# Performance work log

Measured on AMD Instinct MI355X. Metric: run time of the kernel, lower is better.

## Reference

```python
import jax, jax.numpy as jnp
import numpy as np

EPS = 1e-10


def _make_spd(key, shape):
    # entrywise-nonnegative SPD: B>=0 -> B@B^T has nonnegative entries and is PSD;
    # + c*I keeps it well-conditioned and entrywise nonnegative.
    B = jax.random.uniform(key, shape, dtype=jnp.float32)
    D = jnp.einsum('...ij,...kj->...ik', B, B)
    return D + 0.05 * jnp.eye(3, dtype=jnp.float32)


def setup_inputs() -> dict:
    key = jax.random.key(0)
    k1, k2 = jax.random.split(key)
    shape = (2, 128, 128, 64, 3, 3)
    return {"D1": _make_spd(k1, shape), "D2": _make_spd(k2, shape)}


def _log_spd(D):
    # sanitize like torch.nan_to_num(..., nan=eps, posinf=eps, neginf=eps)
    D = jnp.nan_to_num(D, nan=EPS, posinf=EPS, neginf=EPS)
    D = jnp.abs(D)  # entrywise abs; input is symmetric so abs stays symmetric
    w, V = jnp.linalg.eigh(D)            # [...,3], [...,3,3]
    lw = jnp.log(w + EPS) + EPS
    # V @ diag(lw) @ V^T
    return jnp.einsum('...ij,...j,...kj->...ik', V, lw, V)


def reference(D1, D2):
    diff = _log_spd(D1) - _log_spd(D2)
    return jnp.mean(diff * diff)
```

## Files before the change

kernel.cpp:

```cpp
#include <hip/hip_runtime.h>
#include <math.h>

#define EPS_F 1e-10f

typedef __attribute__((ext_vector_type(2))) float f2;
typedef __attribute__((ext_vector_type(2))) unsigned int u2;

__device__ __forceinline__ f2 v_fabs(f2 x) {
  u2 u = __builtin_bit_cast(u2, x);
  u &= 0x7fffffffu;
  return __builtin_bit_cast(f2, u);
}
__device__ __forceinline__ f2 v_max(f2 a, f2 b) { return __builtin_elementwise_max(a, b); }
__device__ __forceinline__ f2 v_min(f2 a, f2 b) { return __builtin_elementwise_min(a, b); }
__device__ __forceinline__ f2 v_log(f2 x) {
  f2 r; r.x = __logf(x.x); r.y = __logf(x.y); return r;
}
__device__ __forceinline__ f2 v_rcp(f2 x) {
  f2 r; r.x = __builtin_amdgcn_rcpf(x.x); r.y = __builtin_amdgcn_rcpf(x.y); return r;
}
__device__ __forceinline__ f2 v_sqrt(f2 x) {
  f2 r; r.x = __builtin_amdgcn_sqrtf(x.x); r.y = __builtin_amdgcn_sqrtf(x.y); return r;
}
__device__ __forceinline__ f2 v_cos(f2 x) {
  f2 r; r.x = __cosf(x.x); r.y = __cosf(x.y); return r;
}

__device__ __forceinline__ f2 v_san(f2 v) {
  f2 a = v_fabs(v);
  f2 r;
  r.x = (a.x <= __FLT_MAX__) ? a.x : EPS_F;
  r.y = (a.y <= __FLT_MAX__) ? a.y : EPS_F;
  return r;
}

__device__ __forceinline__ f2 v_acos(f2 r) {
  const f2 t = v_fabs(r);
  const f2 s = v_sqrt(1.0f - t);
  f2 p = f2{-0.0012624911f, -0.0012624911f};
  p = p * t +  0.0066700901f;
  p = p * t + -0.0170881256f;
  p = p * t +  0.0308918810f;
  p = p * t + -0.0501743046f;
  p = p * t +  0.0889789874f;
  p = p * t + -0.2145988016f;
  p = p * t +  1.5707963050f;
  const f2 ac = s * p;
  f2 res;
  res.x = (r.x < 0.0f) ? (3.14159265358979f - ac.x) : ac.x;
  res.y = (r.y < 0.0f) ? (3.14159265358979f - ac.y) : ac.y;
  return res;
}

__device__ __forceinline__ float pair_loss(f2 a00, f2 a01, f2 a02,
                                           f2 a11, f2 a12, f2 a22) {
  const f2 q   = (a00 + a11 + a22) * (1.0f / 3.0f);
  const f2 b00 = a00 - q, b11 = a11 - q, b22 = a22 - q;
  const f2 p2  = b00 * b00 + b11 * b11 + b22 * b22 +
                 2.0f * (a01 * a01 + a02 * a02 + a12 * a12);

  f2 p = v_sqrt(p2 * (1.0f / 6.0f));
  p = v_max(p, 1e-5f * q + 1e-35f);

  const f2 pinv = v_rcp(p);
  const f2 detB = b00 * (b11 * b22 - a12 * a12)
                - a01 * (a01 * b22 - a12 * a02)
                + a02 * (a01 * a12 - b11 * a02);
  f2 r = detB * 0.5f * pinv * pinv * pinv;
  r = v_min(f2{1.0f, 1.0f}, v_max(f2{-1.0f, -1.0f}, r));
  const f2 phi  = v_acos(r) * (1.0f / 3.0f);
  const f2 twop = 2.0f * p;
  const f2 l1 = q + twop * v_cos(phi);
  const f2 l3 = q + twop * v_cos(phi + 2.0943951023931953f);
  const f2 l2 = 3.0f * q - l1 - l3;

  const f2 s00 = a00 * a00 + a01 * a01 + a02 * a02;
  const f2 s01 = a00 * a01 + a01 * a11 + a02 * a12;
  const f2 s02 = a00 * a02 + a01 * a12 + a02 * a22;
  const f2 s11 = a01 * a01 + a11 * a11 + a12 * a12;
  const f2 s12 = a01 * a02 + a11 * a12 + a12 * a22;
  const f2 s22 = a02 * a02 + a12 * a12 + a22 * a22;

  const f2 g12 = l1 - l2, g23 = l2 - l3;
  f2 alpha, gamma;
  alpha.x = (g12.x >= g23.x) ? l1.x : l3.x;
  gamma.x = (g12.x >= g23.x) ? l3.x : l1.x;
  alpha.y = (g12.y >= g23.y) ? l1.y : l3.y;
  gamma.y = (g12.y >= g23.y) ? l3.y : l1.y;
  const f2 beta = l2;

  const f2 f_a = v_log(alpha + EPS_F) + EPS_F;
  const f2 f_b = v_log(beta  + EPS_F) + EPS_F;
  const f2 f_g = v_log(gamma + EPS_F) + EPS_F;

  const f2 inv_den_a = v_rcp((alpha - beta) * (alpha - gamma));
  const f2 sbg = beta + gamma, pbg = beta * gamma;

  const f2 sab = alpha + beta, pab = alpha * beta;

  const f2 gap = gamma - beta;
  const f2 ga  = gamma - alpha;
  const f2 agap = v_fabs(gap);
  const f2 thr  = 1e-5f * v_max(v_fabs(beta), v_fabs(gamma));
  const f2 mid  = 0.5f * (beta + gamma) + EPS_F;
  f2 num, den;
  num.x = (agap.x > thr.x) ? (f_g.x - f_b.x) : 1.0f;
  den.x = (agap.x > thr.x) ? (gap.x * ga.x) : (mid.x * ga.x);
  num.y = (agap.y > thr.y) ? (f_g.y - f_b.y) : 1.0f;
  den.y = (agap.y > thr.y) ? (gap.y * ga.y) : (mid.y * ga.y);
  const f2 cg = num * v_rcp(den);

  const f2 w = f_a - f_b;
  const f2 wd = w * inv_den_a;

  const f2 L0 = f_b + wd * (s00 - sbg * a00 + pbg) + cg * (s00 - sab * a00 + pab);
  const f2 L1 =       wd * (s01 - sbg * a01)       + cg * (s01 - sab * a01);
  const f2 L2 =       wd * (s02 - sbg * a02)       + cg * (s02 - sab * a02);
  const f2 L3 = f_b + wd * (s11 - sbg * a11 + pbg) + cg * (s11 - sab * a11 + pab);
  const f2 L4 =       wd * (s12 - sbg * a12)       + cg * (s12 - sab * a12);
  const f2 L5 = f_b + wd * (s22 - sbg * a22 + pbg) + cg * (s22 - sab * a22 + pab);

  const float d0 = L0.x - L0.y;
  const float d1 = L1.x - L1.y;
  const float d2 = L2.x - L2.y;
  const float d3 = L3.x - L3.y;
  const float d4 = L4.x - L4.y;
  const float d5 = L5.x - L5.y;
  return d0 * d0 + d3 * d3 + d5 * d5 + 2.0f * (d1 * d1 + d2 * d2 + d4 * d4);
}

#define PAIRS_PER_CHUNK 256
#define FLOATS_PER_CHUNK (PAIRS_PER_CHUNK * 9)

__global__ void __launch_bounds__(256)
leloss_partial(const float* __restrict__ d1, const float* __restrict__ d2,
               float* __restrict__ partial, int nmat, int nchunk) {
  __shared__ float sA[FLOATS_PER_CHUNK];
  __shared__ float sB[FLOATS_PER_CHUNK];

  const int tid = threadIdx.x;
  float acc = 0.0f;

  for (int c = blockIdx.x; c < nchunk; c += gridDim.x) {
    const int base = c * PAIRS_PER_CHUNK;
    const int rem  = nmat - base;

    if (rem >= PAIRS_PER_CHUNK) {
      const float4* g1 = reinterpret_cast<const float4*>(d1 + (size_t)base * 9);
      const float4* g2 = reinterpret_cast<const float4*>(d2 + (size_t)base * 9);
      float4* s4A = reinterpret_cast<float4*>(sA);
      float4* s4B = reinterpret_cast<float4*>(sB);
#pragma unroll
      for (int k = 0; k < FLOATS_PER_CHUNK / 4 / 256 + 1; ++k) {
        const int idx = tid + k * 256;
        if (idx < FLOATS_PER_CHUNK / 4) { s4A[idx] = g1[idx]; s4B[idx] = g2[idx]; }
      }
    } else {
      const int nflt = rem * 9;
      for (int k = tid; k < nflt; k += 256) {
        sA[k] = d1[(size_t)base * 9 + k];
        sB[k] = d2[(size_t)base * 9 + k];
      }
    }
    __syncthreads();

    if (tid < rem) {
      const int o = tid * 9;
      const f2 m00 = v_san(f2{sA[o + 0], sB[o + 0]});
      const f2 m01 = v_san(f2{sA[o + 1], sB[o + 1]});
      const f2 m02 = v_san(f2{sA[o + 2], sB[o + 2]});
      const f2 m11 = v_san(f2{sA[o + 4], sB[o + 4]});
      const f2 m12 = v_san(f2{sA[o + 5], sB[o + 5]});
      const f2 m22 = v_san(f2{sA[o + 8], sB[o + 8]});
      acc += pair_loss(m00, m01, m02, m11, m12, m22);
    }
    __syncthreads();
  }

#pragma unroll
  for (int off = 32; off > 0; off >>= 1) acc += __shfl_down(acc, off, 64);

  __shared__ float wsum[4];
  const int lane = tid & 63;
  const int wid  = tid >> 6;
  if (lane == 0) wsum[wid] = acc;
  __syncthreads();
  if (tid == 0) {
    partial[blockIdx.x] = wsum[0] + wsum[1] + wsum[2] + wsum[3];
  }
}

__global__ void __launch_bounds__(256)
leloss_reduce(const float* __restrict__ partial, int n,
              float* __restrict__ out, double inv_count) {
  double s = 0.0;
  for (int i = threadIdx.x; i < n; i += 256) s += (double)partial[i];
#pragma unroll
  for (int off = 32; off > 0; off >>= 1) s += __shfl_down(s, off, 64);

  __shared__ double wsum[4];
  const int lane = threadIdx.x & 63;
  const int wid  = threadIdx.x >> 6;
  if (lane == 0) wsum[wid] = s;
  __syncthreads();
  if (threadIdx.x == 0) {
    const double total = wsum[0] + wsum[1] + wsum[2] + wsum[3];
    out[0] = (float)(total * inv_count);
  }
}

extern "C" void kernel_launch(void* const* d_in, const int* in_sizes, int n_in,
                              void* d_out, int out_size, void* d_ws, size_t ws_size,
                              hipStream_t stream) {
  const float* d1 = (const float*)d_in[0];
  const float* d2 = (const float*)d_in[1];
  float* out = (float*)d_out;
  float* partial = (float*)d_ws;

  const long long nelem = (long long)in_sizes[0];
  const int nmat   = (int)(nelem / 9);
  const int nchunk = (nmat + PAIRS_PER_CHUNK - 1) / PAIRS_PER_CHUNK;
  const int nblocks = nchunk < 2048 ? nchunk : 2048;

  leloss_partial<<<nblocks, 256, 0, stream>>>(d1, d2, partial, nmat, nchunk);

  const double inv_count = 1.0 / ((double)nmat * 9.0);
  leloss_reduce<<<1, 256, 0, stream>>>(partial, nblocks, out, inv_count);
}
```

Baseline: 33.65 us.

## Load tiles with direct global-to-LDS copies and process two matrix pairs per thread

```diff
diff --git a/kernel.cpp b/kernel.cpp
--- a/kernel.cpp
+++ b/kernel.cpp
@@ -3,41 +3,53 @@
 
 #define EPS_F 1e-10f
 
+typedef __attribute__((ext_vector_type(4))) float f4;
+typedef __attribute__((ext_vector_type(4))) unsigned int u4;
 typedef __attribute__((ext_vector_type(2))) float f2;
-typedef __attribute__((ext_vector_type(2))) unsigned int u2;
-
-__device__ __forceinline__ f2 v_fabs(f2 x) {
-  u2 u = __builtin_bit_cast(u2, x);
+
+typedef const __attribute__((address_space(1))) float4* gv4p;
+typedef __attribute__((address_space(3))) float4* lv4p;
+
+__device__ __forceinline__ f4 v_fabs(f4 x) {
+  u4 u = __builtin_bit_cast(u4, x);
   u &= 0x7fffffffu;
-  return __builtin_bit_cast(f2, u);
-}
-__device__ __forceinline__ f2 v_max(f2 a, f2 b) { return __builtin_elementwise_max(a, b); }
-__device__ __forceinline__ f2 v_min(f2 a, f2 b) { return __builtin_elementwise_min(a, b); }
-__device__ __forceinline__ f2 v_log(f2 x) {
-  f2 r; r.x = __logf(x.x); r.y = __logf(x.y); return r;
-}
-__device__ __forceinline__ f2 v_rcp(f2 x) {
-  f2 r; r.x = __builtin_amdgcn_rcpf(x.x); r.y = __builtin_amdgcn_rcpf(x.y); return r;
-}
-__device__ __forceinline__ f2 v_sqrt(f2 x) {
-  f2 r; r.x = __builtin_amdgcn_sqrtf(x.x); r.y = __builtin_amdgcn_sqrtf(x.y); return r;
-}
-__device__ __forceinline__ f2 v_cos(f2 x) {
-  f2 r; r.x = __cosf(x.x); r.y = __cosf(x.y); return r;
-}
-
-__device__ __forceinline__ f2 v_san(f2 v) {
-  f2 a = v_fabs(v);
-  f2 r;
+  return __builtin_bit_cast(f4, u);
+}
+__device__ __forceinline__ f4 v_max(f4 a, f4 b) { return __builtin_elementwise_max(a, b); }
+__device__ __forceinline__ f4 v_min(f4 a, f4 b) { return __builtin_elementwise_min(a, b); }
+__device__ __forceinline__ f4 v_log(f4 x) {
+  f4 r; r.x = __logf(x.x); r.y = __logf(x.y); r.z = __logf(x.z); r.w = __logf(x.w); return r;
+}
+__device__ __forceinline__ f4 v_rcp(f4 x) {
+  f4 r;
+  r.x = __builtin_amdgcn_rcpf(x.x); r.y = __builtin_amdgcn_rcpf(x.y);
+  r.z = __builtin_amdgcn_rcpf(x.z); r.w = __builtin_amdgcn_rcpf(x.w);
+  return r;
+}
+__device__ __forceinline__ f4 v_sqrt(f4 x) {
+  f4 r;
+  r.x = __builtin_amdgcn_sqrtf(x.x); r.y = __builtin_amdgcn_sqrtf(x.y);
+  r.z = __builtin_amdgcn_sqrtf(x.z); r.w = __builtin_amdgcn_sqrtf(x.w);
+  return r;
+}
+__device__ __forceinline__ f4 v_cos(f4 x) {
+  f4 r; r.x = __cosf(x.x); r.y = __cosf(x.y); r.z = __cosf(x.z); r.w = __cosf(x.w); return r;
+}
+
+__device__ __forceinline__ f4 v_san(f4 v) {
+  f4 a = v_fabs(v);
+  f4 r;
   r.x = (a.x <= __FLT_MAX__) ? a.x : EPS_F;
   r.y = (a.y <= __FLT_MAX__) ? a.y : EPS_F;
+  r.z = (a.z <= __FLT_MAX__) ? a.z : EPS_F;
+  r.w = (a.w <= __FLT_MAX__) ? a.w : EPS_F;
   return r;
 }
 
-__device__ __forceinline__ f2 v_acos(f2 r) {
-  const f2 t = v_fabs(r);
-  const f2 s = v_sqrt(1.0f - t);
-  f2 p = f2{-0.0012624911f, -0.0012624911f};
+__device__ __forceinline__ f4 v_acos(f4 r) {
+  const f4 t = v_fabs(r);
+  const f4 s = v_sqrt(1.0f - t);
+  f4 p = f4{-0.0012624911f, -0.0012624911f, -0.0012624911f, -0.0012624911f};
   p = p * t +  0.0066700901f;
   p = p * t + -0.0170881256f;
   p = p * t +  0.0308918810f;
@@ -45,115 +57,126 @@
   p = p * t +  0.0889789874f;
   p = p * t + -0.2145988016f;
   p = p * t +  1.5707963050f;
-  const f2 ac = s * p;
-  f2 res;
+  const f4 ac = s * p;
+  f4 res;
   res.x = (r.x < 0.0f) ? (3.14159265358979f - ac.x) : ac.x;
   res.y = (r.y < 0.0f) ? (3.14159265358979f - ac.y) : ac.y;
+  res.z = (r.z < 0.0f) ? (3.14159265358979f - ac.z) : ac.z;
+  res.w = (r.w < 0.0f) ? (3.14159265358979f - ac.w) : ac.w;
   return res;
 }
 
-__device__ __forceinline__ float pair_loss(f2 a00, f2 a01, f2 a02,
-                                           f2 a11, f2 a12, f2 a22) {
-  const f2 q   = (a00 + a11 + a22) * (1.0f / 3.0f);
-  const f2 b00 = a00 - q, b11 = a11 - q, b22 = a22 - q;
-  const f2 p2  = b00 * b00 + b11 * b11 + b22 * b22 +
+__device__ __forceinline__ f2 pair_loss(f4 a00, f4 a01, f4 a02,
+                                        f4 a11, f4 a12, f4 a22) {
+  const f4 q   = (a00 + a11 + a22) * (1.0f / 3.0f);
+  const f4 b00 = a00 - q, b11 = a11 - q, b22 = a22 - q;
+  const f4 p2  = b00 * b00 + b11 * b11 + b22 * b22 +
                  2.0f * (a01 * a01 + a02 * a02 + a12 * a12);
 
-  f2 p = v_sqrt(p2 * (1.0f / 6.0f));
+  f4 p = v_sqrt(p2 * (1.0f / 6.0f));
   p = v_max(p, 1e-5f * q + 1e-35f);
 
-  const f2 pinv = v_rcp(p);
-  const f2 detB = b00 * (b11 * b22 - a12 * a12)
+  const f4 pinv = v_rcp(p);
+  const f4 detB = b00 * (b11 * b22 - a12 * a12)
                 - a01 * (a01 * b22 - a12 * a02)
                 + a02 * (a01 * a12 - b11 * a02);
-  f2 r = detB * 0.5f * pinv * pinv * pinv;
-  r = v_min(f2{1.0f, 1.0f}, v_max(f2{-1.0f, -1.0f}, r));
-  const f2 phi  = v_acos(r) * (1.0f / 3.0f);
-  const f2 twop = 2.0f * p;
-  const f2 l1 = q + twop * v_cos(phi);
-  const f2 l3 = q + twop * v_cos(phi + 2.0943951023931953f);
-  const f2 l2 = 3.0f * q - l1 - l3;
-
-  const f2 s00 = a00 * a00 + a01 * a01 + a02 * a02;
-  const f2 s01 = a00 * a01 + a01 * a11 + a02 * a12;
-  const f2 s02 = a00 * a02 + a01 * a12 + a02 * a22;
-  const f2 s11 = a01 * a01 + a11 * a11 + a12 * a12;
-  const f2 s12 = a01 * a02 + a11 * a12 + a12 * a22;
-  const f2 s22 = a02 * a02 + a12 * a12 + a22 * a22;
-
-  const f2 g12 = l1 - l2, g23 = l2 - l3;
-  f2 alpha, gamma;
-  alpha.x = (g12.x >= g23.x) ? l1.x : l3.x;
-  gamma.x = (g12.x >= g23.x) ? l3.x : l1.x;
-  alpha.y = (g12.y >= g23.y) ? l1.y : l3.y;
-  gamma.y = (g12.y >= g23.y) ? l3.y : l1.y;
-  const f2 beta = l2;
-
-  const f2 f_a = v_log(alpha + EPS_F) + EPS_F;
-  const f2 f_b = v_log(beta  + EPS_F) + EPS_F;
-  const f2 f_g = v_log(gamma + EPS_F) + EPS_F;
-
-  const f2 inv_den_a = v_rcp((alpha - beta) * (alpha - gamma));
-  const f2 sbg = beta + gamma, pbg = beta * gamma;
-
-  const f2 sab = alpha + beta, pab = alpha * beta;
-
-  const f2 gap = gamma - beta;
-  const f2 ga  = gamma - alpha;
-  const f2 agap = v_fabs(gap);
-  const f2 thr  = 1e-5f * v_max(v_fabs(beta), v_fabs(gamma));
-  const f2 mid  = 0.5f * (beta + gamma) + EPS_F;
-  f2 num, den;
+  f4 r = detB * 0.5f * pinv * pinv * pinv;
+  r = v_min(f4{1.0f, 1.0f, 1.0f, 1.0f}, v_max(f4{-1.0f, -1.0f, -1.0f, -1.0f}, r));
+  const f4 phi  = v_acos(r) * (1.0f / 3.0f);
+  const f4 twop = 2.0f * p;
+  const f4 l1 = q + twop * v_cos(phi);
+  const f4 l3 = q + twop * v_cos(phi + 2.0943951023931953f);
+  const f4 l2 = 3.0f * q - l1 - l3;
+
+  const f4 s00 = a00 * a00 + a01 * a01 + a02 * a02;
+  const f4 s01 = a00 * a01 + a01 * a11 + a02 * a12;
+  const f4 s02 = a00 * a02 + a01 * a12 + a02 * a22;
+  const f4 s11 = a01 * a01 + a11 * a11 + a12 * a12;
+  const f4 s12 = a01 * a02 + a11 * a12 + a12 * a22;
+  const f4 s22 = a02 * a02 + a12 * a12 + a22 * a22;
+
+  const f4 g12 = l1 - l2, g23 = l2 - l3;
+  f4 alpha, gamma;
+  alpha.x = (g12.x >= g23.x) ? l1.x : l3.x;  gamma.x = (g12.x >= g23.x) ? l3.x : l1.x;
+  alpha.y = (g12.y >= g23.y) ? l1.y : l3.y;  gamma.y = (g12.y >= g23.y) ? l3.y : l1.y;
+  alpha.z = (g12.z >= g23.z) ? l1.z : l3.z;  gamma.z = (g12.z >= g23.z) ? l3.z : l1.z;
+  alpha.w = (g12.w >= g23.w) ? l1.w : l3.w;  gamma.w = (g12.w >= g23.w) ? l3.w : l1.w;
+  const f4 beta = l2;
+
+  const f4 f_a = v_log(alpha + EPS_F) + EPS_F;
+  const f4 f_b = v_log(beta  + EPS_F) + EPS_F;
+  const f4 f_g = v_log(gamma + EPS_F) + EPS_F;
+
+  const f4 inv_den_a = v_rcp((alpha - beta) * (alpha - gamma));
+  const f4 sbg = beta + gamma, pbg = beta * gamma;
+  const f4 sab = alpha + beta, pab = alpha * beta;
+
+  const f4 gap = gamma - beta;
+  const f4 ga  = gamma - alpha;
+  const f4 agap = v_fabs(gap);
+  const f4 thr  = 1e-5f * v_max(v_fabs(beta), v_fabs(gamma));
+  const f4 mid  = 0.5f * (beta + gamma) + EPS_F;
+  f4 num, den;
   num.x = (agap.x > thr.x) ? (f_g.x - f_b.x) : 1.0f;
   den.x = (agap.x > thr.x) ? (gap.x * ga.x) : (mid.x * ga.x);
   num.y = (agap.y > thr.y) ? (f_g.y - f_b.y) : 1.0f;
   den.y = (agap.y > thr.y) ? (gap.y * ga.y) : (mid.y * ga.y);
-  const f2 cg = num * v_rcp(den);
-
-  const f2 w = f_a - f_b;
-  const f2 wd = w * inv_den_a;
-
-  const f2 L0 = f_b + wd * (s00 - sbg * a00 + pbg) + cg * (s00 - sab * a00 + pab);
-  const f2 L1 =       wd * (s01 - sbg * a01)       + cg * (s01 - sab * a01);
-  const f2 L2 =       wd * (s02 - sbg * a02)       + cg * (s02 - sab * a02);
-  const f2 L3 = f_b + wd * (s11 - sbg * a11 + pbg) + cg * (s11 - sab * a11 + pab);
-  const f2 L4 =       wd * (s12 - sbg * a12)       + cg * (s12 - sab * a12);
-  const f2 L5 = f_b + wd * (s22 - sbg * a22 + pbg) + cg * (s22 - sab * a22 + pab);
-
-  const float d0 = L0.x - L0.y;
-  const float d1 = L1.x - L1.y;
-  const float d2 = L2.x - L2.y;
-  const float d3 = L3.x - L3.y;
-  const float d4 = L4.x - L4.y;
-  const float d5 = L5.x - L5.y;
-  return d0 * d0 + d3 * d3 + d5 * d5 + 2.0f * (d1 * d1 + d2 * d2 + d4 * d4);
-}
-
-#define PAIRS_PER_CHUNK 256
-#define FLOATS_PER_CHUNK (PAIRS_PER_CHUNK * 9)
-
-__global__ void __launch_bounds__(256)
+  num.z = (agap.z > thr.z) ? (f_g.z - f_b.z) : 1.0f;
+  den.z = (agap.z > thr.z) ? (gap.z * ga.z) : (mid.z * ga.z);
+  num.w = (agap.w > thr.w) ? (f_g.w - f_b.w) : 1.0f;
+  den.w = (agap.w > thr.w) ? (gap.w * ga.w) : (mid.w * ga.w);
+  const f4 cg = num * v_rcp(den);
+
+  const f4 wd = (f_a - f_b) * inv_den_a;
+
+  const f4 L0 = f_b + wd * (s00 - sbg * a00 + pbg) + cg * (s00 - sab * a00 + pab);
+  const f4 L1 =       wd * (s01 - sbg * a01)       + cg * (s01 - sab * a01);
+  const f4 L2 =       wd * (s02 - sbg * a02)       + cg * (s02 - sab * a02);
+  const f4 L3 = f_b + wd * (s11 - sbg * a11 + pbg) + cg * (s11 - sab * a11 + pab);
+  const f4 L4 =       wd * (s12 - sbg * a12)       + cg * (s12 - sab * a12);
+  const f4 L5 = f_b + wd * (s22 - sbg * a22 + pbg) + cg * (s22 - sab * a22 + pab);
+
+  const float dA0 = L0.x - L0.y, dB0 = L0.z - L0.w;
+  const float dA1 = L1.x - L1.y, dB1 = L1.z - L1.w;
+  const float dA2 = L2.x - L2.y, dB2 = L2.z - L2.w;
+  const float dA3 = L3.x - L3.y, dB3 = L3.z - L3.w;
+  const float dA4 = L4.x - L4.y, dB4 = L4.z - L4.w;
+  const float dA5 = L5.x - L5.y, dB5 = L5.z - L5.w;
+  f2 out;
+  out.x = dA0 * dA0 + dA3 * dA3 + dA5 * dA5 + 2.0f * (dA1 * dA1 + dA2 * dA2 + dA4 * dA4);
+  out.y = dB0 * dB0 + dB3 * dB3 + dB5 * dB5 + 2.0f * (dB1 * dB1 + dB2 * dB2 + dB4 * dB4);
+  return out;
+}
+
+#define CHUNK 512
+#define CHUNK_FLOATS (CHUNK * 9)
+#define CHUNK_V4 (CHUNK_FLOATS / 4)
+
+__global__ void __launch_bounds__(256, 4)
 leloss_partial(const float* __restrict__ d1, const float* __restrict__ d2,
                float* __restrict__ partial, int nmat, int nchunk) {
-  __shared__ float sA[FLOATS_PER_CHUNK];
-  __shared__ float sB[FLOATS_PER_CHUNK];
+  __shared__ float sA[CHUNK_FLOATS];
+  __shared__ float sB[CHUNK_FLOATS];
 
   const int tid = threadIdx.x;
   float acc = 0.0f;
 
   for (int c = blockIdx.x; c < nchunk; c += gridDim.x) {
-    const int base = c * PAIRS_PER_CHUNK;
+    const int base = c * CHUNK;
     const int rem  = nmat - base;
 
-    if (rem >= PAIRS_PER_CHUNK) {
+    if (rem >= CHUNK) {
       const float4* g1 = reinterpret_cast<const float4*>(d1 + (size_t)base * 9);
       const float4* g2 = reinterpret_cast<const float4*>(d2 + (size_t)base * 9);
       float4* s4A = reinterpret_cast<float4*>(sA);
       float4* s4B = reinterpret_cast<float4*>(sB);
 #pragma unroll
-      for (int k = 0; k < FLOATS_PER_CHUNK / 4 / 256 + 1; ++k) {
+      for (int k = 0; k < 5; ++k) {
         const int idx = tid + k * 256;
-        if (idx < FLOATS_PER_CHUNK / 4) { s4A[idx] = g1[idx]; s4B[idx] = g2[idx]; }
+        if (idx < CHUNK_V4) {
+          __builtin_amdgcn_global_load_lds((gv4p)(g1 + idx), (lv4p)(s4A + idx), 16, 0, 0);
+          __builtin_amdgcn_global_load_lds((gv4p)(g2 + idx), (lv4p)(s4B + idx), 16, 0, 0);
+        }
       }
     } else {
       const int nflt = rem * 9;
@@ -164,15 +187,18 @@
     }
     __syncthreads();
 
-    if (tid < rem) {
-      const int o = tid * 9;
-      const f2 m00 = v_san(f2{sA[o + 0], sB[o + 0]});
-      const f2 m01 = v_san(f2{sA[o + 1], sB[o + 1]});
-      const f2 m02 = v_san(f2{sA[o + 2], sB[o + 2]});
-      const f2 m11 = v_san(f2{sA[o + 4], sB[o + 4]});
-      const f2 m12 = v_san(f2{sA[o + 5], sB[o + 5]});
-      const f2 m22 = v_san(f2{sA[o + 8], sB[o + 8]});
-      acc += pair_loss(m00, m01, m02, m11, m12, m22);
+    {
+      const int ia = min(tid, rem - 1);
+      const int ib = min(tid + 256, rem - 1);
+      const int oa = ia * 9, ob = ib * 9;
+      const f4 m00 = v_san(f4{sA[oa + 0], sB[oa + 0], sA[ob + 0], sB[ob + 0]});
+      const f4 m01 = v_san(f4{sA[oa + 1], sB[oa + 1], sA[ob + 1], sB[ob + 1]});
+      const f4 m02 = v_san(f4{sA[oa + 2], sB[oa + 2], sA[ob + 2], sB[ob + 2]});
+      const f4 m11 = v_san(f4{sA[oa + 4], sB[oa + 4], sA[ob + 4], sB[ob + 4]});
+      const f4 m12 = v_san(f4{sA[oa + 5], sB[oa + 5], sA[ob + 5], sB[ob + 5]});
+      const f4 m22 = v_san(f4{sA[oa + 8], sB[oa + 8], sA[ob + 8], sB[ob + 8]});
+      const f2 l = pair_loss(m00, m01, m02, m11, m12, m22);
+      acc += (tid < rem ? l.x : 0.0f) + (tid + 256 < rem ? l.y : 0.0f);
     }
     __syncthreads();
   }
@@ -219,7 +245,7 @@
 
   const long long nelem = (long long)in_sizes[0];
   const int nmat   = (int)(nelem / 9);
-  const int nchunk = (nmat + PAIRS_PER_CHUNK - 1) / PAIRS_PER_CHUNK;
+  const int nchunk = (nmat + CHUNK - 1) / CHUNK;
   const int nblocks = nchunk < 2048 ? nchunk : 2048;
 
   leloss_partial<<<nblocks, 256, 0, stream>>>(d1, d2, partial, nmat, nchunk);
```

Measured after the change: 35.16 us. 1.04x slower.

## Use per-wave direct global-to-LDS loads and simplify log-matrix reconstruction

Applied to the files above, without the earlier changes.

```diff
diff --git a/kernel.cpp b/kernel.cpp
--- a/kernel.cpp
+++ b/kernel.cpp
@@ -5,6 +5,9 @@
 
 typedef __attribute__((ext_vector_type(2))) float f2;
 typedef __attribute__((ext_vector_type(2))) unsigned int u2;
+
+typedef const __attribute__((address_space(1))) char* gcp;
+typedef __attribute__((address_space(3))) char* lcp;
 
 __device__ __forceinline__ f2 v_fabs(f2 x) {
   u2 u = __builtin_bit_cast(u2, x);
@@ -19,19 +22,14 @@
 __device__ __forceinline__ f2 v_rcp(f2 x) {
   f2 r; r.x = __builtin_amdgcn_rcpf(x.x); r.y = __builtin_amdgcn_rcpf(x.y); return r;
 }
+__device__ __forceinline__ f2 v_rsq(f2 x) {
+  f2 r; r.x = __builtin_amdgcn_rsqf(x.x); r.y = __builtin_amdgcn_rsqf(x.y); return r;
+}
 __device__ __forceinline__ f2 v_sqrt(f2 x) {
   f2 r; r.x = __builtin_amdgcn_sqrtf(x.x); r.y = __builtin_amdgcn_sqrtf(x.y); return r;
 }
 __device__ __forceinline__ f2 v_cos(f2 x) {
   f2 r; r.x = __cosf(x.x); r.y = __cosf(x.y); return r;
-}
-
-__device__ __forceinline__ f2 v_san(f2 v) {
-  f2 a = v_fabs(v);
-  f2 r;
-  r.x = (a.x <= __FLT_MAX__) ? a.x : EPS_F;
-  r.y = (a.y <= __FLT_MAX__) ? a.y : EPS_F;
-  return r;
 }
 
 __device__ __forceinline__ f2 v_acos(f2 r) {
@@ -54,15 +52,18 @@
 
 __device__ __forceinline__ float pair_loss(f2 a00, f2 a01, f2 a02,
                                            f2 a11, f2 a12, f2 a22) {
+  a00 = v_fabs(a00); a01 = v_fabs(a01); a02 = v_fabs(a02);
+  a11 = v_fabs(a11); a12 = v_fabs(a12); a22 = v_fabs(a22);
+
   const f2 q   = (a00 + a11 + a22) * (1.0f / 3.0f);
   const f2 b00 = a00 - q, b11 = a11 - q, b22 = a22 - q;
   const f2 p2  = b00 * b00 + b11 * b11 + b22 * b22 +
                  2.0f * (a01 * a01 + a02 * a02 + a12 * a12);
 
-  f2 p = v_sqrt(p2 * (1.0f / 6.0f));
-  p = v_max(p, 1e-5f * q + 1e-35f);
-
-  const f2 pinv = v_rcp(p);
+  const f2 p2c  = v_max(p2 * (1.0f / 6.0f), 1e-10f * q * q + 1e-35f);
+  const f2 pinv = v_rsq(p2c);
+  const f2 p    = p2c * pinv;
+
   const f2 detB = b00 * (b11 * b22 - a12 * a12)
                 - a01 * (a01 * b22 - a12 * a02)
                 + a02 * (a01 * a12 - b11 * a02);
@@ -83,20 +84,15 @@
 
   const f2 g12 = l1 - l2, g23 = l2 - l3;
   f2 alpha, gamma;
-  alpha.x = (g12.x >= g23.x) ? l1.x : l3.x;
-  gamma.x = (g12.x >= g23.x) ? l3.x : l1.x;
-  alpha.y = (g12.y >= g23.y) ? l1.y : l3.y;
-  gamma.y = (g12.y >= g23.y) ? l3.y : l1.y;
+  alpha.x = (g12.x >= g23.x) ? l1.x : l3.x;  gamma.x = (g12.x >= g23.x) ? l3.x : l1.x;
+  alpha.y = (g12.y >= g23.y) ? l1.y : l3.y;  gamma.y = (g12.y >= g23.y) ? l3.y : l1.y;
   const f2 beta = l2;
 
-  const f2 f_a = v_log(alpha + EPS_F) + EPS_F;
-  const f2 f_b = v_log(beta  + EPS_F) + EPS_F;
-  const f2 f_g = v_log(gamma + EPS_F) + EPS_F;
+  const f2 f_a = v_log(alpha + EPS_F);
+  const f2 f_b = v_log(beta  + EPS_F);
+  const f2 f_g = v_log(gamma + EPS_F);
 
   const f2 inv_den_a = v_rcp((alpha - beta) * (alpha - gamma));
-  const f2 sbg = beta + gamma, pbg = beta * gamma;
-
-  const f2 sab = alpha + beta, pab = alpha * beta;
 
   const f2 gap = gamma - beta;
   const f2 ga  = gamma - alpha;
@@ -109,16 +105,20 @@
   num.y = (agap.y > thr.y) ? (f_g.y - f_b.y) : 1.0f;
   den.y = (agap.y > thr.y) ? (gap.y * ga.y) : (mid.y * ga.y);
   const f2 cg = num * v_rcp(den);
-
-  const f2 w = f_a - f_b;
-  const f2 wd = w * inv_den_a;
-
-  const f2 L0 = f_b + wd * (s00 - sbg * a00 + pbg) + cg * (s00 - sab * a00 + pab);
-  const f2 L1 =       wd * (s01 - sbg * a01)       + cg * (s01 - sab * a01);
-  const f2 L2 =       wd * (s02 - sbg * a02)       + cg * (s02 - sab * a02);
-  const f2 L3 = f_b + wd * (s11 - sbg * a11 + pbg) + cg * (s11 - sab * a11 + pab);
-  const f2 L4 =       wd * (s12 - sbg * a12)       + cg * (s12 - sab * a12);
-  const f2 L5 = f_b + wd * (s22 - sbg * a22 + pbg) + cg * (s22 - sab * a22 + pab);
+  const f2 wd = (f_a - f_b) * inv_den_a;
+
+  const f2 sbg = beta + gamma, pbg = beta * gamma;
+  const f2 sab = alpha + beta, pab = alpha * beta;
+  const f2 c2 = wd + cg;
+  const f2 c1 = -(wd * sbg + cg * sab);
+  const f2 c0 = f_b + wd * pbg + cg * pab;
+
+  const f2 L0 = c2 * s00 + c1 * a00 + c0;
+  const f2 L1 = c2 * s01 + c1 * a01;
+  const f2 L2 = c2 * s02 + c1 * a02;
+  const f2 L3 = c2 * s11 + c1 * a11 + c0;
+  const f2 L4 = c2 * s12 + c1 * a12;
+  const f2 L5 = c2 * s22 + c1 * a22 + c0;
 
   const float d0 = L0.x - L0.y;
   const float d1 = L1.x - L1.y;
@@ -129,61 +129,69 @@
   return d0 * d0 + d3 * d3 + d5 * d5 + 2.0f * (d1 * d1 + d2 * d2 + d4 * d4);
 }
 
-#define PAIRS_PER_CHUNK 256
-#define FLOATS_PER_CHUNK (PAIRS_PER_CHUNK * 9)
-
-__global__ void __launch_bounds__(256)
+#define WAVE_BYTES 4608
+#define T_BYTES    2304
+
+__global__ void __launch_bounds__(256, 8)
 leloss_partial(const float* __restrict__ d1, const float* __restrict__ d2,
-               float* __restrict__ partial, int nmat, int nchunk) {
-  __shared__ float sA[FLOATS_PER_CHUNK];
-  __shared__ float sB[FLOATS_PER_CHUNK];
-
-  const int tid = threadIdx.x;
-  float acc = 0.0f;
-
-  for (int c = blockIdx.x; c < nchunk; c += gridDim.x) {
-    const int base = c * PAIRS_PER_CHUNK;
-    const int rem  = nmat - base;
-
-    if (rem >= PAIRS_PER_CHUNK) {
-      const float4* g1 = reinterpret_cast<const float4*>(d1 + (size_t)base * 9);
-      const float4* g2 = reinterpret_cast<const float4*>(d2 + (size_t)base * 9);
-      float4* s4A = reinterpret_cast<float4*>(sA);
-      float4* s4B = reinterpret_cast<float4*>(sB);
-#pragma unroll
-      for (int k = 0; k < FLOATS_PER_CHUNK / 4 / 256 + 1; ++k) {
-        const int idx = tid + k * 256;
-        if (idx < FLOATS_PER_CHUNK / 4) { s4A[idx] = g1[idx]; s4B[idx] = g2[idx]; }
-      }
-    } else {
-      const int nflt = rem * 9;
-      for (int k = tid; k < nflt; k += 256) {
-        sA[k] = d1[(size_t)base * 9 + k];
-        sB[k] = d2[(size_t)base * 9 + k];
-      }
-    }
-    __syncthreads();
-
-    if (tid < rem) {
-      const int o = tid * 9;
-      const f2 m00 = v_san(f2{sA[o + 0], sB[o + 0]});
-      const f2 m01 = v_san(f2{sA[o + 1], sB[o + 1]});
-      const f2 m02 = v_san(f2{sA[o + 2], sB[o + 2]});
-      const f2 m11 = v_san(f2{sA[o + 4], sB[o + 4]});
-      const f2 m12 = v_san(f2{sA[o + 5], sB[o + 5]});
-      const f2 m22 = v_san(f2{sA[o + 8], sB[o + 8]});
-      acc += pair_loss(m00, m01, m02, m11, m12, m22);
-    }
-    __syncthreads();
-  }
-
-#pragma unroll
-  for (int off = 32; off > 0; off >>= 1) acc += __shfl_down(acc, off, 64);
-
-  __shared__ float wsum[4];
+               float* __restrict__ partial, int nmat) {
+  __shared__ float lds[4 * WAVE_BYTES / 4];
+
+  const int tid  = threadIdx.x;
   const int lane = tid & 63;
   const int wid  = tid >> 6;
-  if (lane == 0) wsum[wid] = acc;
+  const int wgid = blockIdx.x * 4 + wid;
+  const int p0   = wgid * 64;
+
+  float acc = 0.0f;
+
+  if (p0 + 64 <= nmat) {
+    const char* s1 = reinterpret_cast<const char*>(d1) + (size_t)p0 * 36;
+    const char* s2 = reinterpret_cast<const char*>(d2) + (size_t)p0 * 36;
+    char* lbase = reinterpret_cast<char*>(lds) + wid * WAVE_BYTES;
+
+#pragma unroll
+    for (int j = 0; j < 4; ++j) {
+      const int o = j * 1024 + lane * 16;
+      const char* src = (o < T_BYTES) ? (s1 + o) : (s2 + (o - T_BYTES));
+      __builtin_amdgcn_global_load_lds((gcp)src, (lcp)(lbase + o), 16, 0, 0);
+    }
+#pragma unroll
+    for (int j = 0; j < 2; ++j) {
+      const int o = 4096 + j * 256 + lane * 4;
+      const char* src = s2 + (o - T_BYTES);
+      __builtin_amdgcn_global_load_lds((gcp)src, (lcp)(lbase + o), 4, 0, 0);
+    }
+    asm volatile("s_waitcnt vmcnt(0)" ::: "memory");
+
+    const float* m1 = lds + wid * (WAVE_BYTES / 4) + lane * 9;
+    const float* m2 = m1 + (T_BYTES / 4);
+    const f2 a00 = f2{m1[0], m2[0]};
+    const f2 a01 = f2{m1[1], m2[1]};
+    const f2 a02 = f2{m1[2], m2[2]};
+    const f2 a11 = f2{m1[4], m2[4]};
+    const f2 a12 = f2{m1[5], m2[5]};
+    const f2 a22 = f2{m1[8], m2[8]};
+    acc = pair_loss(a00, a01, a02, a11, a12, a22);
+  } else {
+    const int pr = p0 + lane;
+    if (pr < nmat) {
+      const size_t base = (size_t)pr * 9;
+      const f2 a00 = f2{d1[base + 0], d2[base + 0]};
+      const f2 a01 = f2{d1[base + 1], d2[base + 1]};
+      const f2 a02 = f2{d1[base + 2], d2[base + 2]};
+      const f2 a11 = f2{d1[base + 4], d2[base + 4]};
+      const f2 a12 = f2{d1[base + 5], d2[base + 5]};
+      const f2 a22 = f2{d1[base + 8], d2[base + 8]};
+      acc = pair_loss(a00, a01, a02, a11, a12, a22);
+    }
+  }
+
+#pragma unroll
+  for (int off = 32; off > 0; off >>= 1) acc += __shfl_down(acc, off, 64);
+
+  __shared__ float wsum[4];
+  if ((tid & 63) == 0) wsum[wid] = acc;
   __syncthreads();
   if (tid == 0) {
     partial[blockIdx.x] = wsum[0] + wsum[1] + wsum[2] + wsum[3];
@@ -218,11 +226,10 @@
   float* partial = (float*)d_ws;
 
   const long long nelem = (long long)in_sizes[0];
-  const int nmat   = (int)(nelem / 9);
-  const int nchunk = (nmat + PAIRS_PER_CHUNK - 1) / PAIRS_PER_CHUNK;
-  const int nblocks = nchunk < 2048 ? nchunk : 2048;
-
-  leloss_partial<<<nblocks, 256, 0, stream>>>(d1, d2, partial, nmat, nchunk);
+  const int nmat = (int)(nelem / 9);
+  const int nblocks = (nmat + 255) / 256;
+
+  leloss_partial<<<nblocks, 256, 0, stream>>>(d1, d2, partial, nmat);
 
   const double inv_count = 1.0 / ((double)nmat * 9.0);
   leloss_reduce<<<1, 256, 0, stream>>>(partial, nblocks, out, inv_count);
```

Result: slower. 38.80 us (+15.3%).
